# Kernel optimization log

Hardware: AMD Instinct MI355X
Metric: run time of the kernel (lower is better)

## Reference

```python
import jax, jax.numpy as jnp
import numpy as np

N_NODES = 100000


def gcn_conv(x, src, dst, W, b):
    # torch_geometric GCNConv: add self-loops, sym-normalize, linear, aggregate
    n = x.shape[0]
    deg = jax.ops.segment_sum(jnp.ones_like(src, dtype=x.dtype), dst, num_segments=n)
    dinv = jnp.where(deg > 0, jax.lax.rsqrt(deg), 0.0)
    norm = dinv[src] * dinv[dst]                      # [E]
    h = x @ W                                         # [N, out]
    msg = h[src] * norm[:, None]                      # [E, out] gather
    out = jax.ops.segment_sum(msg, dst, num_segments=n)  # scatter-add
    return out + b


def add_self_loops(edge_index, n):
    loop = jnp.arange(n, dtype=edge_index.dtype)
    src = jnp.concatenate([edge_index[0], loop])
    dst = jnp.concatenate([edge_index[1], loop])
    return src, dst


def setup_inputs() -> dict:
    key = jax.random.key(0)
    k1, k2, k3, k4 = jax.random.split(key, 4)
    F_in, F_mid = 64, 32
    x = jax.random.normal(k1, (N_NODES, F_in), dtype=jnp.float32)
    edge_index = jax.random.randint(k2, (2, 1200000), 0, N_NODES, dtype=jnp.int64)
    W1 = jax.random.normal(k3, (F_in, F_mid), dtype=jnp.float32) * (1.0 / np.sqrt(F_in))
    b1 = jnp.zeros((F_mid,), dtype=jnp.float32)
    W2 = jax.random.normal(k4, (F_mid, F_in), dtype=jnp.float32) * (1.0 / np.sqrt(F_mid))
    b2 = jnp.zeros((F_in,), dtype=jnp.float32)
    return {"x": x, "edge_index": edge_index, "W1": W1, "b1": b1, "W2": W2, "b2": b2}


def reference(x, edge_index, W1, b1, W2, b2):
    src, dst = add_self_loops(edge_index, x.shape[0])
    h = jax.nn.relu(gcn_conv(x, src, dst, W1, b1))
    # F.dropout in eval mode is identity (module not in training)
    out = gcn_conv(h, src, dst, W2, b2)
    return out
```

## Files before the change

kernel.cpp:

```cpp
#include <hip/hip_runtime.h>


#define CAP 32
#define OVF_MAX 65536
#define SH_BITS 8
#define SH 256
#define BCAP 3584
#define EPB 4096
#define EPT 16

__device__ __forceinline__ unsigned bf16rn(float f) {
    unsigned u = __float_as_uint(f);
    return (u + 0x7fffu + ((u >> 16) & 1u)) >> 16;
}
__device__ __forceinline__ unsigned pack2(float f0, float f1) {
    return (bf16rn(f1) << 16) | bf16rn(f0);
}
__device__ __forceinline__ void acc2(float4& a, uint2 v) {
    a.x += __uint_as_float(v.x << 16);
    a.y += __uint_as_float(v.x & 0xffff0000u);
    a.z += __uint_as_float(v.y << 16);
    a.w += __uint_as_float(v.y & 0xffff0000u);
}

__global__ void init_kernel(int* __restrict__ bcur, int* __restrict__ ovfcnt,
                            unsigned int* __restrict__ g1rowN,
                            unsigned int* __restrict__ q1rowN, int B) {
    int i = blockIdx.x * blockDim.x + threadIdx.x;
    if (i < B) bcur[i] = i * BCAP;
    if (i == 0) *ovfcnt = 0;
    if (i < 16) { g1rowN[i] = 0u; q1rowN[i] = 0u; }
}

__global__ __launch_bounds__(256) void bin_kernel(const int* __restrict__ src,
                                                  const int* __restrict__ dst,
                                                  int* __restrict__ bcur,
                                                  unsigned int* __restrict__ ebuf,
                                                  int* __restrict__ ovfcnt,
                                                  int* __restrict__ ovf, int E, int B) {
    __shared__ int h[512];
    __shared__ int gp[512];
    __shared__ int lr[512];
    for (int b = threadIdx.x; b < B; b += 256) { h[b] = 0; lr[b] = 0; }
    __syncthreads();
    int base = blockIdx.x * EPB;
    int s[EPT], d[EPT], bk[EPT];
#pragma unroll
    for (int k = 0; k < EPT; ++k) {
        int e = base + k * 256 + threadIdx.x;
        bool ok = e < E;
        s[k]  = ok ? src[e] : 0;
        d[k]  = ok ? dst[e] : 0;
        bk[k] = ok ? (d[k] >> SH_BITS) : -1;
        if (ok) atomicAdd(&h[bk[k]], 1);
    }
    __syncthreads();
    for (int b = threadIdx.x; b < B; b += 256)
        if (h[b]) gp[b] = atomicAdd(&bcur[b], h[b]);
    __syncthreads();
#pragma unroll
    for (int k = 0; k < EPT; ++k) {
        if (bk[k] >= 0) {
            int r = atomicAdd(&lr[bk[k]], 1);
            int pos = gp[bk[k]] + r;
            if (pos < (bk[k] + 1) * BCAP)
                ebuf[pos] = ((unsigned)(d[k] & (SH - 1)) << 24) | (unsigned)s[k];
            else { int o = atomicAdd(ovfcnt, 1); if (o < OVF_MAX) { ovf[2 * o] = s[k]; ovf[2 * o + 1] = d[k]; } }
        }
    }
}

__global__ __launch_bounds__(256) void fillb_kernel(const unsigned int* __restrict__ ebuf,
                                                    const int* __restrict__ bcur,
                                                    int* __restrict__ adj,
                                                    float* __restrict__ dinv,
                                                    int* __restrict__ ovfcnt,
                                                    int* __restrict__ ovf, int N) {
    __shared__ int lcnt[SH];
    __shared__ int ladj[SH * CAP];
    int b = blockIdx.x;
    for (int i = threadIdx.x; i < SH; i += 256) lcnt[i] = 0;
    for (int i = threadIdx.x; i < SH * CAP; i += 256) ladj[i] = N;
    __syncthreads();
    int beg = b * BCAP;
    int tot = bcur[b] - beg;
    int m = tot < BCAP ? tot : BCAP;
    for (int i = threadIdx.x; i < m; i += 256) {
        unsigned p = ebuf[beg + i];
        int ld = (int)(p >> 24), sidx = (int)(p & 0xFFFFFF);
        int q = atomicAdd(&lcnt[ld], 1);
        if (q < CAP) ladj[ld * CAP + q] = sidx;
        else { int o = atomicAdd(ovfcnt, 1); if (o < OVF_MAX) { ovf[2 * o] = sidx; ovf[2 * o + 1] = (b << SH_BITS) + ld; } }
    }
    __syncthreads();
    int nb0 = b << SH_BITS;
    const int4* l4 = (const int4*)ladj;
    int4* a4 = (int4*)(adj + (size_t)nb0 * CAP);
    for (int i = threadIdx.x; i < SH * CAP / 4; i += 256) {
        int nd = nb0 + (i * 4) / CAP;
        if (nd < N) a4[i] = l4[i];
    }
    for (int i = threadIdx.x; i < SH; i += 256) {
        int nd = nb0 + i;
        if (nd < N) dinv[nd] = rsqrtf((float)lcnt[i] + 1.0f);
    }
}

__global__ __launch_bounds__(256) void gemm1_kernel(const float* __restrict__ x,
                                                    const float* __restrict__ W1,
                                                    const float* __restrict__ dinv,
                                                    unsigned int* __restrict__ g1, int N) {
    __shared__ float Ws[64 * 32];
    __shared__ float xs[16][64];
    int tid = threadIdx.x;
    const float4* W4 = (const float4*)W1;
    float4* Ws4 = (float4*)Ws;
    for (int i = tid; i < 512; i += 256) Ws4[i] = W4[i];
    int nb = blockIdx.x * 16;
    {
        int ln = tid >> 4, k4 = (tid & 15) * 4;
        int n = nb + ln;
        float4 v = make_float4(0.f, 0.f, 0.f, 0.f);
        if (n < N) v = *(const float4*)(x + (size_t)n * 64 + k4);
        *(float4*)(&xs[ln][k4]) = v;
    }
    __syncthreads();
    int ln = tid >> 4, j = tid & 15;
    int n = nb + ln;
    if (n < N) {
        float s0 = 0.f, s1 = 0.f;
#pragma unroll
        for (int k = 0; k < 64; ++k) {
            float xv = xs[ln][k];
            s0 += xv * Ws[k * 32 + 2 * j];
            s1 += xv * Ws[k * 32 + 2 * j + 1];
        }
        float dv = dinv[n];
        g1[(size_t)n * 16 + j] = pack2(dv * s0, dv * s1);
    }
}

__device__ __forceinline__ float4 gather_row4(const int4* __restrict__ adj4,
                                              const int* __restrict__ ovfcnt,
                                              const int* __restrict__ ovf,
                                              const uint2* __restrict__ g2,
                                              int n, int l, int N) {
    int4 idx = adj4[(size_t)n * 8 + l];
    float4 a = make_float4(0.f, 0.f, 0.f, 0.f);
    uint2 self = g2[(size_t)n * 8 + l];
    {
        int s0  = __shfl(idx.x, 0, 8), s1  = __shfl(idx.y, 0, 8);
        int s2  = __shfl(idx.z, 0, 8), s3  = __shfl(idx.w, 0, 8);
        int s4  = __shfl(idx.x, 1, 8), s5  = __shfl(idx.y, 1, 8);
        int s6  = __shfl(idx.z, 1, 8), s7  = __shfl(idx.w, 1, 8);
        int s8  = __shfl(idx.x, 2, 8), s9  = __shfl(idx.y, 2, 8);
        int s10 = __shfl(idx.z, 2, 8), s11 = __shfl(idx.w, 2, 8);
        int s12 = __shfl(idx.x, 3, 8), s13 = __shfl(idx.y, 3, 8);
        int s14 = __shfl(idx.z, 3, 8), s15 = __shfl(idx.w, 3, 8);
        uint2 v0  = g2[(size_t)s0  * 8 + l], v1  = g2[(size_t)s1  * 8 + l];
        uint2 v2  = g2[(size_t)s2  * 8 + l], v3  = g2[(size_t)s3  * 8 + l];
        uint2 v4  = g2[(size_t)s4  * 8 + l], v5  = g2[(size_t)s5  * 8 + l];
        uint2 v6  = g2[(size_t)s6  * 8 + l], v7  = g2[(size_t)s7  * 8 + l];
        uint2 v8  = g2[(size_t)s8  * 8 + l], v9  = g2[(size_t)s9  * 8 + l];
        uint2 v10 = g2[(size_t)s10 * 8 + l], v11 = g2[(size_t)s11 * 8 + l];
        uint2 v12 = g2[(size_t)s12 * 8 + l], v13 = g2[(size_t)s13 * 8 + l];
        uint2 v14 = g2[(size_t)s14 * 8 + l], v15 = g2[(size_t)s15 * 8 + l];
        acc2(a, self);
        acc2(a, v0);  acc2(a, v1);  acc2(a, v2);  acc2(a, v3);
        acc2(a, v4);  acc2(a, v5);  acc2(a, v6);  acc2(a, v7);
        acc2(a, v8);  acc2(a, v9);  acc2(a, v10); acc2(a, v11);
        acc2(a, v12); acc2(a, v13); acc2(a, v14); acc2(a, v15);
    }
    if (__shfl(idx.x, 4, 8) != N) {
        int s0  = __shfl(idx.x, 4, 8), s1  = __shfl(idx.y, 4, 8);
        int s2  = __shfl(idx.z, 4, 8), s3  = __shfl(idx.w, 4, 8);
        int s4  = __shfl(idx.x, 5, 8), s5  = __shfl(idx.y, 5, 8);
        int s6  = __shfl(idx.z, 5, 8), s7  = __shfl(idx.w, 5, 8);
        int s8  = __shfl(idx.x, 6, 8), s9  = __shfl(idx.y, 6, 8);
        int s10 = __shfl(idx.z, 6, 8), s11 = __shfl(idx.w, 6, 8);
        int s12 = __shfl(idx.x, 7, 8), s13 = __shfl(idx.y, 7, 8);
        int s14 = __shfl(idx.z, 7, 8), s15 = __shfl(idx.w, 7, 8);
        uint2 v0  = g2[(size_t)s0  * 8 + l], v1  = g2[(size_t)s1  * 8 + l];
        uint2 v2  = g2[(size_t)s2  * 8 + l], v3  = g2[(size_t)s3  * 8 + l];
        uint2 v4  = g2[(size_t)s4  * 8 + l], v5  = g2[(size_t)s5  * 8 + l];
        uint2 v6  = g2[(size_t)s6  * 8 + l], v7  = g2[(size_t)s7  * 8 + l];
        uint2 v8  = g2[(size_t)s8  * 8 + l], v9  = g2[(size_t)s9  * 8 + l];
        uint2 v10 = g2[(size_t)s10 * 8 + l], v11 = g2[(size_t)s11 * 8 + l];
        uint2 v12 = g2[(size_t)s12 * 8 + l], v13 = g2[(size_t)s13 * 8 + l];
        uint2 v14 = g2[(size_t)s14 * 8 + l], v15 = g2[(size_t)s15 * 8 + l];
        acc2(a, v0);  acc2(a, v1);  acc2(a, v2);  acc2(a, v3);
        acc2(a, v4);  acc2(a, v5);  acc2(a, v6);  acc2(a, v7);
        acc2(a, v8);  acc2(a, v9);  acc2(a, v10); acc2(a, v11);
        acc2(a, v12); acc2(a, v13); acc2(a, v14); acc2(a, v15);
    }
    int c = *ovfcnt; if (c > OVF_MAX) c = OVF_MAX;
    for (int i = 0; i < c; ++i) {
        if (ovf[2 * i + 1] == n) acc2(a, g2[(size_t)ovf[2 * i] * 8 + l]);
    }
    return a;
}

__global__ void gather_q_kernel(const int4* __restrict__ adj4,
                                const int* __restrict__ ovfcnt, const int* __restrict__ ovf,
                                const uint2* __restrict__ g2, const float* __restrict__ dinv,
                                const float* __restrict__ b1, uint2* __restrict__ q2, int N) {
    int tid = blockIdx.x * blockDim.x + threadIdx.x;
    int n = tid >> 3, l = tid & 7;
    if (n < N) {
        float4 a = gather_row4(adj4, ovfcnt, ovf, g2, n, l, N);
        float dv = dinv[n];
        float4 bb = ((const float4*)b1)[l];
        float vx = dv * a.x + bb.x, vy = dv * a.y + bb.y;
        float vz = dv * a.z + bb.z, vw = dv * a.w + bb.w;
        vx = vx > 0.f ? vx : 0.f; vy = vy > 0.f ? vy : 0.f;
        vz = vz > 0.f ? vz : 0.f; vw = vw > 0.f ? vw : 0.f;
        q2[(size_t)n * 8 + l] = make_uint2(pack2(dv * vx, dv * vy), pack2(dv * vz, dv * vw));
    }
}

__global__ __launch_bounds__(256) void gather_out_kernel(
        const int4* __restrict__ adj4,
        const int* __restrict__ ovfcnt, const int* __restrict__ ovf,
        const uint2* __restrict__ q2, const float* __restrict__ dinv,
        const float* __restrict__ W2, const float* __restrict__ b2,
        float* __restrict__ out, int N) {
    __shared__ float Ws[32 * 64];
    __shared__ float sAgg[32][36];
    int tid = threadIdx.x;
    const float4* W4 = (const float4*)W2;
    float4* Ws4 = (float4*)Ws;
    for (int i = tid; i < 512; i += 256) Ws4[i] = W4[i];
    int nb = blockIdx.x * 32;
    int o = tid >> 3, l = tid & 7;
    int n = nb + o;
    if (n < N) *(float4*)(&sAgg[o][l * 4]) = gather_row4(adj4, ovfcnt, ovf, q2, n, l, N);
    __syncthreads();
    int ln = tid >> 6, j = tid & 63;
#pragma unroll
    for (int nn = 0; nn < 8; ++nn) {
        int ol = nn * 4 + ln;
        int node = nb + ol;
        if (node < N) {
            float s = 0.f;
#pragma unroll
            for (int k = 0; k < 32; ++k) s += sAgg[ol][k] * Ws[k * 64 + j];
            out[(size_t)node * 64 + j] = dinv[node] * s + b2[j];
        }
    }
}

extern "C" void kernel_launch(void* const* d_in, const int* in_sizes, int n_in,
                              void* d_out, int out_size, void* d_ws, size_t ws_size,
                              hipStream_t stream) {
    const float* x  = (const float*)d_in[0];
    const int*   ei = (const int*)d_in[1];
    const float* W1 = (const float*)d_in[2];
    const float* b1 = (const float*)d_in[3];
    const float* W2 = (const float*)d_in[4];
    const float* b2 = (const float*)d_in[5];
    float* out = (float*)d_out;

    int N = in_sizes[0] / 64;
    int E = in_sizes[1] / 2;
    const int* src = ei;
    const int* dst = ei + (size_t)E;
    int B = (N + SH - 1) >> SH_BITS;

    size_t NP = (size_t)N + 1;
    float* dinv   = (float*)d_ws;
    unsigned int* g1 = (unsigned int*)(dinv + N);
    unsigned int* q1 = g1 + 16 * NP;
    unsigned int* ebuf = q1;
    int*   adj    = (int*)(q1 + 16 * NP);
    int*   bcur   = adj + (size_t)CAP * N;
    int*   ovfcnt = bcur + 512;
    int*   ovf    = ovfcnt + 4;

    init_kernel<<<(B + 255) / 256, 256, 0, stream>>>(bcur, ovfcnt,
                                                     g1 + 16 * (size_t)N, q1 + 16 * (size_t)N, B);
    bin_kernel<<<(E + EPB - 1) / EPB, 256, 0, stream>>>(src, dst, bcur, ebuf, ovfcnt, ovf, E, B);
    fillb_kernel<<<B, 256, 0, stream>>>(ebuf, bcur, adj, dinv, ovfcnt, ovf, N);

    gemm1_kernel<<<(N + 15) / 16, 256, 0, stream>>>(x, W1, dinv, g1, N);

    long long tq = (long long)N * 8;
    gather_q_kernel<<<(int)((tq + 255) / 256), 256, 0, stream>>>(
        (const int4*)adj, ovfcnt, ovf, (const uint2*)g1, dinv, b1, (uint2*)q1, N);
    gather_out_kernel<<<(N + 31) / 32, 256, 0, stream>>>(
        (const int4*)adj, ovfcnt, ovf, (const uint2*)q1, dinv, W2, b2, out, N);
}
```

Measured before the change: 179.0 us.

## Replace two-pass binned adjacency build with direct global-atomic per-node fill

Removes the bin/fill two-stage construction that staged edges through shared-memory buckets, replacing it with one kernel where each edge atomically increments a per-node counter in global memory and writes its source into a fixed-capacity adjacency slot. The adjacency array is prefilled with a sentinel in the init kernel, and dinv is now computed inside gemm1 from the counts. This drops one kernel launch and the intermediate edge buffer, but relies on scattered global atomics and uncoalesced writes over 1.2M edges. The overflow capacity is also reduced, which may drop edges for high-degree nodes.

Measured after the change: 252.7 us. 41.2% more time.

```diff
diff --git a/kernel.cpp b/kernel.cpp
--- a/kernel.cpp
+++ b/kernel.cpp
@@ -2,12 +2,7 @@
 
 
 #define CAP 32
-#define OVF_MAX 65536
-#define SH_BITS 8
-#define SH 256
-#define BCAP 3584
-#define EPB 4096
-#define EPT 16
+#define OVF_MAX 4096
 
 __device__ __forceinline__ unsigned bf16rn(float f) {
     unsigned u = __float_as_uint(f);
@@ -23,92 +18,43 @@
     a.w += __uint_as_float(v.y & 0xffff0000u);
 }
 
-__global__ void init_kernel(int* __restrict__ bcur, int* __restrict__ ovfcnt,
-                            unsigned int* __restrict__ g1rowN,
-                            unsigned int* __restrict__ q1rowN, int B) {
+__global__ __launch_bounds__(256) void init_kernel(int4* __restrict__ adj4,
+                                                   int* __restrict__ cnt,
+                                                   int* __restrict__ ovfcnt,
+                                                   unsigned int* __restrict__ g1rowN,
+                                                   unsigned int* __restrict__ q1rowN, int N) {
     int i = blockIdx.x * blockDim.x + threadIdx.x;
-    if (i < B) bcur[i] = i * BCAP;
+    int NA = 8 * N;
+    if (i < NA) adj4[i] = make_int4(N, N, N, N);
+    if (i < N) cnt[i] = 0;
     if (i == 0) *ovfcnt = 0;
     if (i < 16) { g1rowN[i] = 0u; q1rowN[i] = 0u; }
 }
 
-__global__ __launch_bounds__(256) void bin_kernel(const int* __restrict__ src,
-                                                  const int* __restrict__ dst,
-                                                  int* __restrict__ bcur,
-                                                  unsigned int* __restrict__ ebuf,
-                                                  int* __restrict__ ovfcnt,
-                                                  int* __restrict__ ovf, int E, int B) {
-    __shared__ int h[512];
-    __shared__ int gp[512];
-    __shared__ int lr[512];
-    for (int b = threadIdx.x; b < B; b += 256) { h[b] = 0; lr[b] = 0; }
-    __syncthreads();
-    int base = blockIdx.x * EPB;
-    int s[EPT], d[EPT], bk[EPT];
-#pragma unroll
-    for (int k = 0; k < EPT; ++k) {
-        int e = base + k * 256 + threadIdx.x;
-        bool ok = e < E;
-        s[k]  = ok ? src[e] : 0;
-        d[k]  = ok ? dst[e] : 0;
-        bk[k] = ok ? (d[k] >> SH_BITS) : -1;
-        if (ok) atomicAdd(&h[bk[k]], 1);
-    }
-    __syncthreads();
-    for (int b = threadIdx.x; b < B; b += 256)
-        if (h[b]) gp[b] = atomicAdd(&bcur[b], h[b]);
-    __syncthreads();
-#pragma unroll
-    for (int k = 0; k < EPT; ++k) {
-        if (bk[k] >= 0) {
-            int r = atomicAdd(&lr[bk[k]], 1);
-            int pos = gp[bk[k]] + r;
-            if (pos < (bk[k] + 1) * BCAP)
-                ebuf[pos] = ((unsigned)(d[k] & (SH - 1)) << 24) | (unsigned)s[k];
-            else { int o = atomicAdd(ovfcnt, 1); if (o < OVF_MAX) { ovf[2 * o] = s[k]; ovf[2 * o + 1] = d[k]; } }
+__global__ __launch_bounds__(256) void build_kernel(const int* __restrict__ src,
+                                                    const int* __restrict__ dst,
+                                                    int* __restrict__ cnt,
+                                                    int* __restrict__ adj,
+                                                    int* __restrict__ ovfcnt,
+                                                    int* __restrict__ ovf, int E, int N) {
+    int e = blockIdx.x * blockDim.x + threadIdx.x;
+    if (e < E) {
+        int s = src[e], d = dst[e];
+        if ((unsigned)d < (unsigned)N && (unsigned)s < (unsigned)N) {
+            int q = atomicAdd(&cnt[d], 1);
+            if (q < CAP) adj[(size_t)d * CAP + q] = s;
+            else {
+                int o = atomicAdd(ovfcnt, 1);
+                if (o < OVF_MAX) { ovf[2 * o] = s; ovf[2 * o + 1] = d; }
+            }
         }
-    }
-}
-
-__global__ __launch_bounds__(256) void fillb_kernel(const unsigned int* __restrict__ ebuf,
-                                                    const int* __restrict__ bcur,
-                                                    int* __restrict__ adj,
-                                                    float* __restrict__ dinv,
-                                                    int* __restrict__ ovfcnt,
-                                                    int* __restrict__ ovf, int N) {
-    __shared__ int lcnt[SH];
-    __shared__ int ladj[SH * CAP];
-    int b = blockIdx.x;
-    for (int i = threadIdx.x; i < SH; i += 256) lcnt[i] = 0;
-    for (int i = threadIdx.x; i < SH * CAP; i += 256) ladj[i] = N;
-    __syncthreads();
-    int beg = b * BCAP;
-    int tot = bcur[b] - beg;
-    int m = tot < BCAP ? tot : BCAP;
-    for (int i = threadIdx.x; i < m; i += 256) {
-        unsigned p = ebuf[beg + i];
-        int ld = (int)(p >> 24), sidx = (int)(p & 0xFFFFFF);
-        int q = atomicAdd(&lcnt[ld], 1);
-        if (q < CAP) ladj[ld * CAP + q] = sidx;
-        else { int o = atomicAdd(ovfcnt, 1); if (o < OVF_MAX) { ovf[2 * o] = sidx; ovf[2 * o + 1] = (b << SH_BITS) + ld; } }
-    }
-    __syncthreads();
-    int nb0 = b << SH_BITS;
-    const int4* l4 = (const int4*)ladj;
-    int4* a4 = (int4*)(adj + (size_t)nb0 * CAP);
-    for (int i = threadIdx.x; i < SH * CAP / 4; i += 256) {
-        int nd = nb0 + (i * 4) / CAP;
-        if (nd < N) a4[i] = l4[i];
-    }
-    for (int i = threadIdx.x; i < SH; i += 256) {
-        int nd = nb0 + i;
-        if (nd < N) dinv[nd] = rsqrtf((float)lcnt[i] + 1.0f);
     }
 }
 
 __global__ __launch_bounds__(256) void gemm1_kernel(const float* __restrict__ x,
                                                     const float* __restrict__ W1,
-                                                    const float* __restrict__ dinv,
+                                                    const int* __restrict__ cnt,
+                                                    float* __restrict__ dinv,
                                                     unsigned int* __restrict__ g1, int N) {
     __shared__ float Ws[64 * 32];
     __shared__ float xs[16][64];
@@ -135,7 +81,8 @@
             s0 += xv * Ws[k * 32 + 2 * j];
             s1 += xv * Ws[k * 32 + 2 * j + 1];
         }
-        float dv = dinv[n];
+        float dv = rsqrtf((float)cnt[n] + 1.0f);
+        if (j == 0) dinv[n] = dv;
         g1[(size_t)n * 16 + j] = pack2(dv * s0, dv * s1);
     }
 }
@@ -264,24 +211,22 @@
     int E = in_sizes[1] / 2;
     const int* src = ei;
     const int* dst = ei + (size_t)E;
-    int B = (N + SH - 1) >> SH_BITS;
 
     size_t NP = (size_t)N + 1;
     float* dinv   = (float*)d_ws;
     unsigned int* g1 = (unsigned int*)(dinv + N);
     unsigned int* q1 = g1 + 16 * NP;
-    unsigned int* ebuf = q1;
     int*   adj    = (int*)(q1 + 16 * NP);
-    int*   bcur   = adj + (size_t)CAP * N;
-    int*   ovfcnt = bcur + 512;
+    int*   cnt    = adj + (size_t)CAP * N;
+    int*   ovfcnt = cnt + N;
     int*   ovf    = ovfcnt + 4;
 
-    init_kernel<<<(B + 255) / 256, 256, 0, stream>>>(bcur, ovfcnt,
-                                                     g1 + 16 * (size_t)N, q1 + 16 * (size_t)N, B);
-    bin_kernel<<<(E + EPB - 1) / EPB, 256, 0, stream>>>(src, dst, bcur, ebuf, ovfcnt, ovf, E, B);
-    fillb_kernel<<<B, 256, 0, stream>>>(ebuf, bcur, adj, dinv, ovfcnt, ovf, N);
-
-    gemm1_kernel<<<(N + 15) / 16, 256, 0, stream>>>(x, W1, dinv, g1, N);
+    int NA = 8 * N;
+    init_kernel<<<(NA + 255) / 256, 256, 0, stream>>>(
+        (int4*)adj, cnt, ovfcnt, g1 + 16 * (size_t)N, q1 + 16 * (size_t)N, N);
+    build_kernel<<<(E + 255) / 256, 256, 0, stream>>>(src, dst, cnt, adj, ovfcnt, ovf, E, N);
+
+    gemm1_kernel<<<(N + 15) / 16, 256, 0, stream>>>(x, W1, cnt, dinv, g1, N);
 
     long long tq = (long long)N * 8;
     gather_q_kernel<<<(int)((tq + 255) / 256), 256, 0, stream>>>(
```
